# Optimization experiments

Measured on AMD Instinct MI355X. Metric: run time of the kernel, lower is better.

The kernel has to match this reference:

```python
import jax, jax.numpy as jnp
import numpy as np

GAMMA = 0.99
LAMBDA = 0.95
NU = 0.001
LOG_2PI = float(np.log(2.0 * np.pi))

B, T, H, R, C, A = 256, 64, 512, 32, 32, 64
H1, H2 = 1024, 1024
D = H + R * C  # critic input dim = hidden_state + flattened latent


def setup_inputs() -> dict:
    key = jax.random.key(0)
    ks = jax.random.split(key, 13)
    sc = lambda n: 1.0 / np.sqrt(n)
    return {
        "h": jax.random.normal(ks[0], (B, T, H), jnp.float32),
        "z": jax.random.normal(ks[1], (B, T, R, C), jnp.float32),
        "reward": jax.random.normal(ks[2], (B, T, 1), jnp.float32) * 0.1,
        "cont": jax.random.uniform(ks[3], (B, T, 1), jnp.float32),
        "action": jax.random.normal(ks[4], (B, T, A), jnp.float32),
        "a_mu": jax.random.normal(ks[5], (B, T, A), jnp.float32),
        "a_sigma": jax.random.uniform(ks[6], (B, T, A), jnp.float32) + 0.5,
        "W1": jax.random.normal(ks[7], (D, H1), jnp.float32) * sc(D),
        "b1": jnp.zeros((H1,), jnp.float32),
        "W2": jax.random.normal(ks[8], (H1, H2), jnp.float32) * sc(H1),
        "b2": jnp.zeros((H2,), jnp.float32),
        "W3": jax.random.normal(ks[9], (H2, 1), jnp.float32) * sc(H2),
        "b3": jnp.zeros((1,), jnp.float32),
    }


def _critic(h, z, W1, b1, W2, b2, W3, b3):
    # flatten latent [B,T,R,C] -> [B,T,R*C], concat with hidden state
    zf = z.reshape(z.shape[0], z.shape[1], -1)
    st = jnp.concatenate([h, zf], axis=-1)  # [B,T,D]
    x = jax.nn.silu(st @ W1 + b1)
    x = jax.nn.silu(x @ W2 + b2)
    return x @ W3 + b3  # [B,T,1]


def _r_lambda(value, reward, cont):
    # value/reward/cont: [B,T,1]; backward TD(lambda) recursion over time
    vt = value[..., 0].T   # [T,B] time-major
    rt = reward[..., 0].T
    ct = cont[..., 0].T

    def step(R_next, xs):
        r, c, v_next = xs
        R_cur = r + GAMMA * c * ((1.0 - LAMBDA) * v_next + LAMBDA * R_next)
        return R_cur, R_cur

    _, Rs = jax.lax.scan(step, vt[-1], (rt[:-1], ct[:-1], vt[1:]), reverse=True)
    R_lam = jnp.concatenate([Rs, vt[-1:]], axis=0)  # [T,B]
    return R_lam.T[..., None]  # [B,T,1]


def reference(h, z, reward, cont, action, a_mu, a_sigma, W1, b1, W2, b2, W3, b3):
    value = _critic(h, z, W1, b1, W2, b2, W3, b3)  # [B,T,1]
    # R_lambda uses detached value estimates
    R_lam = _r_lambda(jax.lax.stop_gradient(value), reward, cont)  # [B,T,1]
    advantage = R_lam - value  # [B,T,1]

    # Normal(mu, sigma) log_prob and entropy
    log_sig = jnp.log(a_sigma)
    log_prob = -0.5 * jnp.square((action - a_mu) / a_sigma) - log_sig - 0.5 * LOG_2PI  # [B,T,A]
    entropy = 0.5 + 0.5 * LOG_2PI + log_sig  # [B,T,A]

    loss_actor = -jnp.mean(
        log_prob * jax.lax.stop_gradient(advantage)
        + NU * jax.lax.stop_gradient(entropy)
    )
    loss_critic = jnp.mean(0.5 * jnp.square(value - jax.lax.stop_gradient(R_lam)))
    return jnp.stack([loss_actor, loss_critic])
```

## Files before the change

kernel.cpp:

```cpp
#include <hip/hip_runtime.h>
#include <hip/hip_bf16.h>
#include <stdint.h>

typedef short s8v  __attribute__((ext_vector_type(8)));
typedef float f4v  __attribute__((ext_vector_type(4)));

__device__ __forceinline__ unsigned short f2bf(float f) {
  unsigned int u = __float_as_uint(f);
  u += 0x7fffu + ((u >> 16) & 1u);
  return (unsigned short)(u >> 16);
}

#define GLOAD16(g, l)                                                          \
  __builtin_amdgcn_global_load_lds(                                            \
      (const __attribute__((address_space(1))) unsigned int*)(g),              \
      (__attribute__((address_space(3))) unsigned int*)(l), 16, 0, 0)

__global__ __launch_bounds__(256) void prep_x(const float* __restrict__ h,
                                              const float* __restrict__ z,
                                              unsigned short* __restrict__ X) {
  int idx = blockIdx.x * 256 + threadIdx.x;
  int m = idx / 192;
  int c = (idx - m * 192) * 8;
  const float* s = (c < 512) ? (h + (size_t)m * 512 + c)
                             : (z + (size_t)m * 1024 + (c - 512));
  f4v f0 = *(const f4v*)s;
  f4v f1 = *(const f4v*)(s + 4);
  s8v o;
  o[0] = (short)f2bf(f0[0]); o[1] = (short)f2bf(f0[1]);
  o[2] = (short)f2bf(f0[2]); o[3] = (short)f2bf(f0[3]);
  o[4] = (short)f2bf(f1[0]); o[5] = (short)f2bf(f1[1]);
  o[6] = (short)f2bf(f1[2]); o[7] = (short)f2bf(f1[3]);
  *(s8v*)(X + (size_t)m * 1536 + c) = o;
}

__global__ __launch_bounds__(256) void transpose_w(const float* __restrict__ W,
                                                   unsigned short* __restrict__ WT,
                                                   int K, int N) {
  __shared__ float tile[32][33];
  int tx = threadIdx.x & 31;
  int ty = threadIdx.x >> 5;
  int k0 = blockIdx.x * 32;
  int n0 = blockIdx.y * 32;
#pragma unroll
  for (int i = 0; i < 4; ++i)
    tile[ty + i * 8][tx] = W[(size_t)(k0 + ty + i * 8) * N + n0 + tx];
  __syncthreads();
#pragma unroll
  for (int i = 0; i < 4; ++i)
    WT[(size_t)(n0 + ty + i * 8) * K + k0 + tx] = f2bf(tile[tx][ty + i * 8]);
}

template<int K, bool FUSE>
__global__ __launch_bounds__(512) void gemm256(
    const unsigned short* __restrict__ A, const unsigned short* __restrict__ Bt,
    const float* __restrict__ bias, unsigned short* __restrict__ Cout,
    const float* __restrict__ W3, float* __restrict__ value) {
  constexpr int NOUT = 1024;
  constexpr int NT = K / 32;
  __shared__ char lds[131072];

  const int tid = threadIdx.x;
  const int w = tid >> 6, l = tid & 63;
  const int wr = w >> 2, wc = w & 3;
  const int tm = blockIdx.x * 256;
  const int tn = blockIdx.y * 256;
  const int l15 = l & 15, lh = l >> 4;

  const int ul   = (tid & 7) ^ ((tid >> 3) & 7);
  const int srow = ((tid >> 3) << 1) + (ul >> 2);
  const int sk   = (ul & 3) * 8;
  const unsigned short* Ag = A  + (size_t)(tm + srow) * K + sk;
  const unsigned short* Bg = Bt + (size_t)(tn + srow) * K + sk;
  const int wb = w * 1024;

  const int ra = wr * 128 + l15;
  const int rb = wc * 64 + l15;
  const int aoff = (ra >> 1) * 128 + (((((ra & 1) << 2) | lh) ^ ((ra >> 1) & 7)) << 4);
  const int boff = 16384 + (rb >> 1) * 128 + (((((rb & 1) << 2) | lh) ^ ((rb >> 1) & 7)) << 4);

  f4v acc[8][4];
#pragma unroll
  for (int i = 0; i < 8; ++i)
#pragma unroll
    for (int j = 0; j < 4; ++j) acc[i][j] = (f4v){0.f, 0.f, 0.f, 0.f};

  auto stage = [&](int t) {
    char* d = lds + (t & 3) * 32768 + wb;
    const int kt = t * 32;
    GLOAD16(Ag + kt, d);
    GLOAD16(Ag + (size_t)128 * K + kt, d + 8192);
    GLOAD16(Bg + kt, d + 16384);
    GLOAD16(Bg + (size_t)128 * K + kt, d + 24576);
  };

  stage(0); stage(1); stage(2);

#define MFMA4(mi, av)                                                          \
  acc[mi][0] = __builtin_amdgcn_mfma_f32_16x16x32_bf16(av, bf0, acc[mi][0], 0, 0, 0); \
  acc[mi][1] = __builtin_amdgcn_mfma_f32_16x16x32_bf16(av, bf1, acc[mi][1], 0, 0, 0); \
  acc[mi][2] = __builtin_amdgcn_mfma_f32_16x16x32_bf16(av, bf2, acc[mi][2], 0, 0, 0); \
  acc[mi][3] = __builtin_amdgcn_mfma_f32_16x16x32_bf16(av, bf3, acc[mi][3], 0, 0, 0);

#define TILE(t, VM)                                                            \
  {                                                                            \
    asm volatile(VM ::: "memory");                                             \
    __builtin_amdgcn_s_barrier();                                              \
    char* const sb = lds + ((t) & 3) * 32768;                                  \
    s8v bf0 = *(const s8v*)(sb + boff);                                        \
    s8v bf1 = *(const s8v*)(sb + boff + 1024);                                 \
    s8v bf2 = *(const s8v*)(sb + boff + 2048);                                 \
    s8v bf3 = *(const s8v*)(sb + boff + 3072);                                 \
    s8v a0 = *(const s8v*)(sb + aoff);                                         \
    s8v a1 = *(const s8v*)(sb + aoff + 1024);                                  \
    s8v a2 = *(const s8v*)(sb + aoff + 2048);                                  \
    s8v a3 = *(const s8v*)(sb + aoff + 3072);                                  \
    if ((t) + 3 < NT) stage((t) + 3);                                          \
    __builtin_amdgcn_s_setprio(1);                                             \
    MFMA4(0, a0) MFMA4(1, a1) MFMA4(2, a2) MFMA4(3, a3)                        \
    __builtin_amdgcn_s_setprio(0);                                             \
    a0 = *(const s8v*)(sb + aoff + 4096);                                      \
    a1 = *(const s8v*)(sb + aoff + 5120);                                      \
    a2 = *(const s8v*)(sb + aoff + 6144);                                      \
    a3 = *(const s8v*)(sb + aoff + 7168);                                      \
    __builtin_amdgcn_s_setprio(1);                                             \
    MFMA4(4, a0) MFMA4(5, a1) MFMA4(6, a2) MFMA4(7, a3)                        \
    __builtin_amdgcn_s_setprio(0);                                             \
  }

  for (int t = 0; t < NT - 2; ++t) TILE(t, "s_waitcnt vmcnt(8)")
  TILE(NT - 2, "s_waitcnt vmcnt(4)")
  TILE(NT - 1, "s_waitcnt vmcnt(0)")

#undef TILE
#undef MFMA4

  if constexpr (!FUSE) {
#pragma unroll
    for (int ni = 0; ni < 4; ++ni) {
      const int col = tn + wc * 64 + ni * 16 + l15;
      const float bb = bias[col];
#pragma unroll
      for (int mi = 0; mi < 8; ++mi) {
#pragma unroll
        for (int r = 0; r < 4; ++r) {
          const int row = tm + wr * 128 + mi * 16 + lh * 4 + r;
          float v = acc[mi][ni][r] + bb;
          v = v / (1.f + __expf(-v));
          Cout[(size_t)row * NOUT + col] = f2bf(v);
        }
      }
    }
  } else {
    float bb[4], w3[4];
#pragma unroll
    for (int ni = 0; ni < 4; ++ni) {
      const int col = tn + wc * 64 + ni * 16 + l15;
      bb[ni] = bias[col];
      w3[ni] = W3[col];
    }
#pragma unroll
    for (int mi = 0; mi < 8; ++mi) {
#pragma unroll
      for (int r = 0; r < 4; ++r) {
        float s = 0.f;
#pragma unroll
        for (int ni = 0; ni < 4; ++ni) {
          float v = acc[mi][ni][r] + bb[ni];
          v = v / (1.f + __expf(-v));
          s += v * w3[ni];
        }
        s += __shfl_xor(s, 1);
        s += __shfl_xor(s, 2);
        s += __shfl_xor(s, 4);
        s += __shfl_xor(s, 8);
        if (l15 == 0)
          atomicAdd(&value[tm + wr * 128 + mi * 16 + lh * 4 + r], s);
      }
    }
  }
}

__global__ __launch_bounds__(256) void td_actor(
    const float* __restrict__ value, const float* __restrict__ reward,
    const float* __restrict__ cont, const float* __restrict__ b3,
    const float* __restrict__ action, const float* __restrict__ a_mu,
    const float* __restrict__ a_sigma, float* __restrict__ accs) {
  __shared__ float vv[64], rr[64], cc[64], adv_s[64];
  const int b = blockIdx.x, tid = threadIdx.x;
  if (tid < 64) {
    vv[tid] = value[b * 64 + tid] + b3[0];
    rr[tid] = reward[b * 64 + tid];
    cc[tid] = cont[b * 64 + tid];
  }
  __syncthreads();
  if (tid == 0) {
    const float g = 0.99f, lam = 0.95f;
    float Rn = vv[63];
    adv_s[63] = 0.f;
    float s2 = 0.f;
    for (int t = 62; t >= 0; --t) {
      float R = rr[t] + g * cc[t] * ((1.f - lam) * vv[t + 1] + lam * Rn);
      float a = R - vv[t];
      adv_s[t] = a;
      s2 += a * a;
      Rn = R;
    }
    atomicAdd(&accs[0], s2);
  }
  __syncthreads();
  const float C1 = 0.91893853320467274f;
  const float NU = 0.001f;
  const float av = adv_s[tid >> 2];
  const size_t base = (size_t)b * 4096 + tid * 16;
  float s = 0.f;
#pragma unroll
  for (int j = 0; j < 4; ++j) {
    f4v a  = *(const f4v*)(action  + base + j * 4);
    f4v mu = *(const f4v*)(a_mu    + base + j * 4);
    f4v sg = *(const f4v*)(a_sigma + base + j * 4);
#pragma unroll
    for (int i = 0; i < 4; ++i) {
      float d = (a[i] - mu[i]) / sg[i];
      float ls = __logf(sg[i]);
      float lp = -0.5f * d * d - ls - C1;
      s += lp * av + NU * (0.5f + C1 + ls);
    }
  }
#pragma unroll
  for (int off = 32; off; off >>= 1) s += __shfl_down(s, off);
  __shared__ float red[4];
  if ((tid & 63) == 0) red[tid >> 6] = s;
  __syncthreads();
  if (tid == 0) atomicAdd(&accs[1], red[0] + red[1] + red[2] + red[3]);
}

__global__ void fin_kernel(const float* __restrict__ accs, float* __restrict__ out) {
  out[0] = -accs[1] / 1048576.0f;
  out[1] = 0.5f * accs[0] / 16384.0f;
}

extern "C" void kernel_launch(void* const* d_in, const int* in_sizes, int n_in,
                              void* d_out, int out_size, void* d_ws, size_t ws_size,
                              hipStream_t stream) {
  const float* h       = (const float*)d_in[0];
  const float* z       = (const float*)d_in[1];
  const float* reward  = (const float*)d_in[2];
  const float* cont    = (const float*)d_in[3];
  const float* action  = (const float*)d_in[4];
  const float* a_mu    = (const float*)d_in[5];
  const float* a_sigma = (const float*)d_in[6];
  const float* W1      = (const float*)d_in[7];
  const float* b1      = (const float*)d_in[8];
  const float* W2      = (const float*)d_in[9];
  const float* b2      = (const float*)d_in[10];
  const float* W3      = (const float*)d_in[11];
  const float* b3      = (const float*)d_in[12];

  char* ws = (char*)d_ws;
  unsigned short* X   = (unsigned short*)(ws);
  unsigned short* W1T = (unsigned short*)(ws + 50331648);
  unsigned short* W2T = (unsigned short*)(ws + 53477376);
  unsigned short* X1  = (unsigned short*)(ws + 55574528);
  float* value = (float*)(ws + 89128960);
  float* accs  = (float*)(ws + 89194496);

  hipMemsetAsync(value, 0, 65552, stream);
  prep_x<<<12288, 256, 0, stream>>>(h, z, X);
  transpose_w<<<dim3(48, 32), 256, 0, stream>>>(W1, W1T, 1536, 1024);
  transpose_w<<<dim3(32, 32), 256, 0, stream>>>(W2, W2T, 1024, 1024);
  gemm256<1536, false><<<dim3(64, 4), 512, 0, stream>>>(X, W1T, b1, X1, nullptr, nullptr);
  gemm256<1024, true><<<dim3(64, 4), 512, 0, stream>>>(X1, W2T, b2, nullptr, W3, value);
  td_actor<<<256, 256, 0, stream>>>(value, reward, cont, b3, action, a_mu, a_sigma, accs);
  fin_kernel<<<1, 1, 0, stream>>>(accs, (float*)d_out);
}
```

Measured before the change: 265.3 us.

## Shrink GEMM tiles to 128x256, merge prep kernels, drop memset and global atomics

The GEMMs now use 128x256 tiles with triple buffering in 72KB of LDS, which doubles the grid to 512 blocks and should give better CU coverage on the device. The three prep kernels are merged into one launch. The hipMemsetAsync is removed: value partials are written per column-block after reducing in LDS, and per-batch loss partials are written to an array that a 256-thread final kernel reduces. The smaller tiles halve A-tile reuse per block and give a shallower pipeline.

```diff
diff --git a/kernel.cpp b/kernel.cpp
--- a/kernel.cpp
+++ b/kernel.cpp
@@ -16,35 +16,41 @@
       (const __attribute__((address_space(1))) unsigned int*)(g),              \
       (__attribute__((address_space(3))) unsigned int*)(l), 16, 0, 0)
 
-__global__ __launch_bounds__(256) void prep_x(const float* __restrict__ h,
-                                              const float* __restrict__ z,
-                                              unsigned short* __restrict__ X) {
-  int idx = blockIdx.x * 256 + threadIdx.x;
-  int m = idx / 192;
-  int c = (idx - m * 192) * 8;
-  const float* s = (c < 512) ? (h + (size_t)m * 512 + c)
-                             : (z + (size_t)m * 1024 + (c - 512));
-  f4v f0 = *(const f4v*)s;
-  f4v f1 = *(const f4v*)(s + 4);
-  s8v o;
-  o[0] = (short)f2bf(f0[0]); o[1] = (short)f2bf(f0[1]);
-  o[2] = (short)f2bf(f0[2]); o[3] = (short)f2bf(f0[3]);
-  o[4] = (short)f2bf(f1[0]); o[5] = (short)f2bf(f1[1]);
-  o[6] = (short)f2bf(f1[2]); o[7] = (short)f2bf(f1[3]);
-  *(s8v*)(X + (size_t)m * 1536 + c) = o;
-}
-
-__global__ __launch_bounds__(256) void transpose_w(const float* __restrict__ W,
-                                                   unsigned short* __restrict__ WT,
-                                                   int K, int N) {
+__global__ __launch_bounds__(256) void prep_all(
+    const float* __restrict__ h, const float* __restrict__ z,
+    unsigned short* __restrict__ X,
+    const float* __restrict__ W1, unsigned short* __restrict__ W1T,
+    const float* __restrict__ W2, unsigned short* __restrict__ W2T) {
   __shared__ float tile[32][33];
-  int tx = threadIdx.x & 31;
-  int ty = threadIdx.x >> 5;
-  int k0 = blockIdx.x * 32;
-  int n0 = blockIdx.y * 32;
+  const int bid = blockIdx.x, tid = threadIdx.x;
+  if (bid < 12288) {
+    int idx = bid * 256 + tid;
+    int m = idx / 192;
+    int c = (idx - m * 192) * 8;
+    const float* s = (c < 512) ? (h + (size_t)m * 512 + c)
+                               : (z + (size_t)m * 1024 + (c - 512));
+    f4v f0 = *(const f4v*)s;
+    f4v f1 = *(const f4v*)(s + 4);
+    s8v o;
+    o[0] = (short)f2bf(f0[0]); o[1] = (short)f2bf(f0[1]);
+    o[2] = (short)f2bf(f0[2]); o[3] = (short)f2bf(f0[3]);
+    o[4] = (short)f2bf(f1[0]); o[5] = (short)f2bf(f1[1]);
+    o[6] = (short)f2bf(f1[2]); o[7] = (short)f2bf(f1[3]);
+    *(s8v*)(X + (size_t)m * 1536 + c) = o;
+    return;
+  }
+  const float* W;
+  unsigned short* WT;
+  int K, loc;
+  if (bid < 13824) { W = W1; WT = W1T; K = 1536; loc = bid - 12288;
+  } else           { W = W2; WT = W2T; K = 1024; loc = bid - 13824; }
+  const int kt = (K == 1536) ? (loc % 48) : (loc % 32);
+  const int nt = (K == 1536) ? (loc / 48) : (loc / 32);
+  const int k0 = kt * 32, n0 = nt * 32;
+  const int tx = tid & 31, ty = tid >> 5;
 #pragma unroll
   for (int i = 0; i < 4; ++i)
-    tile[ty + i * 8][tx] = W[(size_t)(k0 + ty + i * 8) * N + n0 + tx];
+    tile[ty + i * 8][tx] = W[(size_t)(k0 + ty + i * 8) * 1024 + n0 + tx];
   __syncthreads();
 #pragma unroll
   for (int i = 0; i < 4; ++i)
@@ -52,18 +58,17 @@
 }
 
 template<int K, bool FUSE>
-__global__ __launch_bounds__(512) void gemm256(
+__global__ __launch_bounds__(512, 4) void gemm128(
     const unsigned short* __restrict__ A, const unsigned short* __restrict__ Bt,
     const float* __restrict__ bias, unsigned short* __restrict__ Cout,
-    const float* __restrict__ W3, float* __restrict__ value) {
-  constexpr int NOUT = 1024;
+    const float* __restrict__ W3, float* __restrict__ value_part) {
   constexpr int NT = K / 32;
-  __shared__ char lds[131072];
+  __shared__ char lds[73728];
 
   const int tid = threadIdx.x;
   const int w = tid >> 6, l = tid & 63;
   const int wr = w >> 2, wc = w & 3;
-  const int tm = blockIdx.x * 256;
+  const int tm = blockIdx.x * 128;
   const int tn = blockIdx.y * 256;
   const int l15 = l & 15, lh = l >> 4;
 
@@ -74,27 +79,26 @@
   const unsigned short* Bg = Bt + (size_t)(tn + srow) * K + sk;
   const int wb = w * 1024;
 
-  const int ra = wr * 128 + l15;
+  const int ra = wr * 64 + l15;
   const int rb = wc * 64 + l15;
   const int aoff = (ra >> 1) * 128 + (((((ra & 1) << 2) | lh) ^ ((ra >> 1) & 7)) << 4);
-  const int boff = 16384 + (rb >> 1) * 128 + (((((rb & 1) << 2) | lh) ^ ((rb >> 1) & 7)) << 4);
-
-  f4v acc[8][4];
-#pragma unroll
-  for (int i = 0; i < 8; ++i)
+  const int boff = 8192 + (rb >> 1) * 128 + (((((rb & 1) << 2) | lh) ^ ((rb >> 1) & 7)) << 4);
+
+  f4v acc[4][4];
+#pragma unroll
+  for (int i = 0; i < 4; ++i)
 #pragma unroll
     for (int j = 0; j < 4; ++j) acc[i][j] = (f4v){0.f, 0.f, 0.f, 0.f};
 
-  auto stage = [&](int t) {
-    char* d = lds + (t & 3) * 32768 + wb;
+  auto stage = [&](int t, int so) {
+    char* d = lds + so + wb;
     const int kt = t * 32;
     GLOAD16(Ag + kt, d);
-    GLOAD16(Ag + (size_t)128 * K + kt, d + 8192);
-    GLOAD16(Bg + kt, d + 16384);
-    GLOAD16(Bg + (size_t)128 * K + kt, d + 24576);
+    GLOAD16(Bg + kt, d + 8192);
+    GLOAD16(Bg + (size_t)128 * K + kt, d + 16384);
   };
 
-  stage(0); stage(1); stage(2);
+  stage(0, 0); stage(1, 24576);
 
 #define MFMA4(mi, av)                                                          \
   acc[mi][0] = __builtin_amdgcn_mfma_f32_16x16x32_bf16(av, bf0, acc[mi][0], 0, 0, 0); \
@@ -102,52 +106,54 @@
   acc[mi][2] = __builtin_amdgcn_mfma_f32_16x16x32_bf16(av, bf2, acc[mi][2], 0, 0, 0); \
   acc[mi][3] = __builtin_amdgcn_mfma_f32_16x16x32_bf16(av, bf3, acc[mi][3], 0, 0, 0);
 
-#define TILE(t, VM)                                                            \
+#define TILE(t, coff, soff, ST, VM)                                            \
   {                                                                            \
     asm volatile(VM ::: "memory");                                             \
     __builtin_amdgcn_s_barrier();                                              \
-    char* const sb = lds + ((t) & 3) * 32768;                                  \
+    char* const sb = lds + (coff);                                             \
     s8v bf0 = *(const s8v*)(sb + boff);                                        \
     s8v bf1 = *(const s8v*)(sb + boff + 1024);                                 \
     s8v bf2 = *(const s8v*)(sb + boff + 2048);                                 \
     s8v bf3 = *(const s8v*)(sb + boff + 3072);                                 \
     s8v a0 = *(const s8v*)(sb + aoff);                                         \
     s8v a1 = *(const s8v*)(sb + aoff + 1024);                                  \
-    s8v a2 = *(const s8v*)(sb + aoff + 2048);                                  \
-    s8v a3 = *(const s8v*)(sb + aoff + 3072);                                  \
-    if ((t) + 3 < NT) stage((t) + 3);                                          \
+    if (ST) stage((t) + 2, (soff));                                            \
     __builtin_amdgcn_s_setprio(1);                                             \
-    MFMA4(0, a0) MFMA4(1, a1) MFMA4(2, a2) MFMA4(3, a3)                        \
+    MFMA4(0, a0) MFMA4(1, a1)                                                  \
     __builtin_amdgcn_s_setprio(0);                                             \
-    a0 = *(const s8v*)(sb + aoff + 4096);                                      \
-    a1 = *(const s8v*)(sb + aoff + 5120);                                      \
-    a2 = *(const s8v*)(sb + aoff + 6144);                                      \
-    a3 = *(const s8v*)(sb + aoff + 7168);                                      \
+    a0 = *(const s8v*)(sb + aoff + 2048);                                      \
+    a1 = *(const s8v*)(sb + aoff + 3072);                                      \
     __builtin_amdgcn_s_setprio(1);                                             \
-    MFMA4(4, a0) MFMA4(5, a1) MFMA4(6, a2) MFMA4(7, a3)                        \
+    MFMA4(2, a0) MFMA4(3, a1)                                                  \
     __builtin_amdgcn_s_setprio(0);                                             \
   }
 
-  for (int t = 0; t < NT - 2; ++t) TILE(t, "s_waitcnt vmcnt(8)")
-  TILE(NT - 2, "s_waitcnt vmcnt(4)")
-  TILE(NT - 1, "s_waitcnt vmcnt(0)")
+  int coff = 0, soff = 49152;
+  for (int t = 0; t < NT - 1; ++t) {
+    TILE(t, coff, soff, (t + 2 < NT), "s_waitcnt vmcnt(3)")
+    coff = (coff == 49152) ? 0 : coff + 24576;
+    soff = (soff == 49152) ? 0 : soff + 24576;
+  }
+  TILE(NT - 1, coff, 0, false, "s_waitcnt vmcnt(0)")
 
 #undef TILE
 #undef MFMA4
 
   if constexpr (!FUSE) {
-#pragma unroll
-    for (int ni = 0; ni < 4; ++ni) {
-      const int col = tn + wc * 64 + ni * 16 + l15;
-      const float bb = bias[col];
-#pragma unroll
-      for (int mi = 0; mi < 8; ++mi) {
-#pragma unroll
-        for (int r = 0; r < 4; ++r) {
-          const int row = tm + wr * 128 + mi * 16 + lh * 4 + r;
-          float v = acc[mi][ni][r] + bb;
+    float bb[4];
+#pragma unroll
+    for (int ni = 0; ni < 4; ++ni) bb[ni] = bias[tn + wc * 64 + ni * 16 + l15];
+#pragma unroll
+    for (int mi = 0; mi < 4; ++mi) {
+#pragma unroll
+      for (int r = 0; r < 4; ++r) {
+        const int row = tm + wr * 64 + mi * 16 + lh * 4 + r;
+#pragma unroll
+        for (int ni = 0; ni < 4; ++ni) {
+          const int col = tn + wc * 64 + ni * 16 + l15;
+          float v = acc[mi][ni][r] + bb[ni];
           v = v / (1.f + __expf(-v));
-          Cout[(size_t)row * NOUT + col] = f2bf(v);
+          Cout[(size_t)row * 1024 + col] = f2bf(v);
         }
       }
     }
@@ -159,8 +165,12 @@
       bb[ni] = bias[col];
       w3[ni] = W3[col];
     }
-#pragma unroll
-    for (int mi = 0; mi < 8; ++mi) {
+    float* vpart = (float*)lds;
+    __syncthreads();
+    if (tid < 128) vpart[tid] = 0.f;
+    __syncthreads();
+#pragma unroll
+    for (int mi = 0; mi < 4; ++mi) {
 #pragma unroll
       for (int r = 0; r < 4; ++r) {
         float s = 0.f;
@@ -175,23 +185,28 @@
         s += __shfl_xor(s, 4);
         s += __shfl_xor(s, 8);
         if (l15 == 0)
-          atomicAdd(&value[tm + wr * 128 + mi * 16 + lh * 4 + r], s);
+          atomicAdd(&vpart[wr * 64 + mi * 16 + lh * 4 + r], s);
       }
     }
+    __syncthreads();
+    if (tid < 128)
+      value_part[(size_t)blockIdx.y * 16384 + tm + tid] = vpart[tid];
   }
 }
 
 __global__ __launch_bounds__(256) void td_actor(
-    const float* __restrict__ value, const float* __restrict__ reward,
+    const float* __restrict__ value_part, const float* __restrict__ reward,
     const float* __restrict__ cont, const float* __restrict__ b3,
     const float* __restrict__ action, const float* __restrict__ a_mu,
-    const float* __restrict__ a_sigma, float* __restrict__ accs) {
+    const float* __restrict__ a_sigma, float* __restrict__ accs_arr) {
   __shared__ float vv[64], rr[64], cc[64], adv_s[64];
   const int b = blockIdx.x, tid = threadIdx.x;
   if (tid < 64) {
-    vv[tid] = value[b * 64 + tid] + b3[0];
-    rr[tid] = reward[b * 64 + tid];
-    cc[tid] = cont[b * 64 + tid];
+    const int i = b * 64 + tid;
+    vv[tid] = value_part[i] + value_part[16384 + i] + value_part[32768 + i] +
+              value_part[49152 + i] + b3[0];
+    rr[tid] = reward[i];
+    cc[tid] = cont[i];
   }
   __syncthreads();
   if (tid == 0) {
@@ -206,7 +221,7 @@
       s2 += a * a;
       Rn = R;
     }
-    atomicAdd(&accs[0], s2);
+    accs_arr[b * 2] = s2;
   }
   __syncthreads();
   const float C1 = 0.91893853320467274f;
@@ -232,12 +247,26 @@
   __shared__ float red[4];
   if ((tid & 63) == 0) red[tid >> 6] = s;
   __syncthreads();
-  if (tid == 0) atomicAdd(&accs[1], red[0] + red[1] + red[2] + red[3]);
-}
-
-__global__ void fin_kernel(const float* __restrict__ accs, float* __restrict__ out) {
-  out[0] = -accs[1] / 1048576.0f;
-  out[1] = 0.5f * accs[0] / 16384.0f;
+  if (tid == 0) accs_arr[b * 2 + 1] = red[0] + red[1] + red[2] + red[3];
+}
+
+__global__ __launch_bounds__(256) void fin_kernel(
+    const float* __restrict__ accs_arr, float* __restrict__ out) {
+  const int tid = threadIdx.x;
+  float c = accs_arr[tid * 2];
+  float a = accs_arr[tid * 2 + 1];
+#pragma unroll
+  for (int off = 32; off; off >>= 1) {
+    c += __shfl_down(c, off);
+    a += __shfl_down(a, off);
+  }
+  __shared__ float rc[4], ra[4];
+  if ((tid & 63) == 0) { rc[tid >> 6] = c; ra[tid >> 6] = a; }
+  __syncthreads();
+  if (tid == 0) {
+    out[0] = -(ra[0] + ra[1] + ra[2] + ra[3]) / 1048576.0f;
+    out[1] = 0.5f * (rc[0] + rc[1] + rc[2] + rc[3]) / 16384.0f;
+  }
 }
 
 extern "C" void kernel_launch(void* const* d_in, const int* in_sizes, int n_in,
@@ -258,19 +287,16 @@
   const float* b3      = (const float*)d_in[12];
 
   char* ws = (char*)d_ws;
-  unsigned short* X   = (unsigned short*)(ws);
-  unsigned short* W1T = (unsigned short*)(ws + 50331648);
-  unsigned short* W2T = (unsigned short*)(ws + 53477376);
-  unsigned short* X1  = (unsigned short*)(ws + 55574528);
-  float* value = (float*)(ws + 89128960);
-  float* accs  = (float*)(ws + 89194496);
-
-  hipMemsetAsync(value, 0, 65552, stream);
-  prep_x<<<12288, 256, 0, stream>>>(h, z, X);
-  transpose_w<<<dim3(48, 32), 256, 0, stream>>>(W1, W1T, 1536, 1024);
-  transpose_w<<<dim3(32, 32), 256, 0, stream>>>(W2, W2T, 1024, 1024);
-  gemm256<1536, false><<<dim3(64, 4), 512, 0, stream>>>(X, W1T, b1, X1, nullptr, nullptr);
-  gemm256<1024, true><<<dim3(64, 4), 512, 0, stream>>>(X1, W2T, b2, nullptr, W3, value);
-  td_actor<<<256, 256, 0, stream>>>(value, reward, cont, b3, action, a_mu, a_sigma, accs);
-  fin_kernel<<<1, 1, 0, stream>>>(accs, (float*)d_out);
-}
+  unsigned short* X    = (unsigned short*)(ws);
+  unsigned short* W1T  = (unsigned short*)(ws + 50331648);
+  unsigned short* W2T  = (unsigned short*)(ws + 53477376);
+  unsigned short* X1   = (unsigned short*)(ws + 55574528);
+  float* value_part    = (float*)(ws + 89128960);
+  float* accs_arr      = (float*)(ws + 89391104);
+
+  prep_all<<<14848, 256, 0, stream>>>(h, z, X, W1, W1T, W2, W2T);
+  gemm128<1536, false><<<dim3(128, 4), 512, 0, stream>>>(X, W1T, b1, X1, nullptr, nullptr);
+  gemm128<1024, true><<<dim3(128, 4), 512, 0, stream>>>(X1, W2T, b2, nullptr, W3, value_part);
+  td_actor<<<256, 256, 0, stream>>>(value_part, reward, cont, b3, action, a_mu, a_sigma, accs_arr);
+  fin_kernel<<<1, 256, 0, stream>>>(accs_arr, (float*)d_out);
+}
```

Result: no change. 261.1 us (-1.6%).
